# Kernel optimization log

Measured on AMD Instinct MI355X. Metric: run time of the kernel, lower is better.

Reference implementation:

```python
import jax, jax.numpy as jnp
import numpy as np

NUM_CAMS, NUM_LEVELS, NUM_PTS, NUM_GROUPS = 6, 4, 13, 8


def grid_sample(fm, grid):
    """Bilinear grid_sample, align_corners=False, zeros padding.
    fm: (N,C,H,W); grid: (N,P,Q,2) xy in [-1,1] -> (N,C,P,Q)."""
    N, C, H, W = fm.shape
    x, y = grid[..., 0], grid[..., 1]
    ix = ((x + 1.0) * W - 1.0) * 0.5
    iy = ((y + 1.0) * H - 1.0) * 0.5
    ix0f = jnp.floor(ix)
    iy0f = jnp.floor(iy)
    wx1 = ix - ix0f
    wy1 = iy - iy0f
    wx0 = 1.0 - wx1
    wy0 = 1.0 - wy1
    ix0 = ix0f.astype(jnp.int32)
    iy0 = iy0f.astype(jnp.int32)
    flat = fm.reshape(N, C, H * W)

    def gather(iyc, ixc):
        valid = ((ixc >= 0) & (ixc < W) & (iyc >= 0) & (iyc < H)).astype(fm.dtype)
        idx = jnp.clip(iyc, 0, H - 1) * W + jnp.clip(ixc, 0, W - 1)
        g = jnp.take_along_axis(flat, idx.reshape(N, 1, -1), axis=2)
        return g.reshape((N, C) + idx.shape[1:]) * valid[:, None]

    v00 = gather(iy0, ix0)
    v01 = gather(iy0, ix0 + 1)
    v10 = gather(iy0 + 1, ix0)
    v11 = gather(iy0 + 1, ix0 + 1)
    return (v00 * (wy0 * wx0)[:, None] + v01 * (wy0 * wx1)[:, None]
            + v10 * (wy1 * wx0)[:, None] + v11 * (wy1 * wx1)[:, None])


def setup_inputs() -> dict:
    key = jax.random.key(0)
    ks = jax.random.split(key, 16)
    bs, NA, E = 2, 900, 256
    shapes = [(12, E, 64, 176), (12, E, 32, 88), (12, E, 16, 44), (12, E, 8, 22)]
    proj = jnp.eye(4, dtype=jnp.float32)[None, None] + 0.1 * jax.random.normal(ks[0], (bs, NUM_CAMS, 4, 4), jnp.float32)
    return {
        "instance_feature": jax.random.normal(ks[1], (bs, NA, E), jnp.float32),
        "anchor": jax.random.normal(ks[2], (bs, NA, E), jnp.float32),
        "anchor_embed": jax.random.normal(ks[3], (bs, NA, E), jnp.float32),
        "fm0": jax.random.normal(ks[4], shapes[0], jnp.float32),
        "fm1": jax.random.normal(ks[5], shapes[1], jnp.float32),
        "fm2": jax.random.normal(ks[6], shapes[2], jnp.float32),
        "fm3": jax.random.normal(ks[7], shapes[3], jnp.float32),
        "projection_mat": proj,
        "W_kps": 0.02 * jax.random.normal(ks[8], (E, NUM_PTS * 3), jnp.float32),
        "b_kps": jnp.zeros((NUM_PTS * 3,), jnp.float32),
        "W_wfc": 0.02 * jax.random.normal(ks[9], (E, NUM_GROUPS * NUM_CAMS * NUM_LEVELS * NUM_PTS), jnp.float32),
        "b_wfc": jnp.zeros((NUM_GROUPS * NUM_CAMS * NUM_LEVELS * NUM_PTS,), jnp.float32),
        "W_out": 0.02 * jax.random.normal(ks[10], (E, E), jnp.float32),
        "b_out": jnp.zeros((E,), jnp.float32),
    }


def reference(instance_feature, anchor, anchor_embed, fm0, fm1, fm2, fm3,
              projection_mat, W_kps, b_kps, W_wfc, b_wfc, W_out, b_out):
    bs, NA, E = instance_feature.shape
    C, L, P, G = NUM_CAMS, NUM_LEVELS, NUM_PTS, NUM_GROUPS
    gd = E // G
    # key points: anchor center + learned offsets (kps_generator)
    offs = (instance_feature @ W_kps + b_kps).reshape(bs, NA, P, 3)
    key_points = anchor[:, :, None, :3] + offs  # (bs,NA,P,3)
    # fusion weights: softmax over cam*level*pt slots, per group
    feat = instance_feature + anchor_embed
    w = (feat @ W_wfc + b_wfc).reshape(bs, NA, C * L * P, G)
    w = jax.nn.softmax(w, axis=-2)
    # project points to 2D
    pts = jnp.concatenate([key_points, jnp.ones_like(key_points[..., :1])], axis=-1)
    p2d = jnp.einsum('bcij,bnpj->bcnpi', projection_mat, pts)  # (bs,C,NA,P,4)
    depth = 1.0 / jnp.clip(p2d[..., 2:3], 1e-5)
    grid = (p2d[..., :2] * depth).reshape(bs * C, NA, P, 2)
    # multi-level bilinear sampling
    samples = [grid_sample(fm, grid) for fm in (fm0, fm1, fm2, fm3)]  # (bs*C,E,NA,P)
    feats = jnp.concatenate(samples, axis=3)  # (bs*C,E,NA,L*P)
    feats = feats.reshape(bs, C, E, NA, L * P).transpose(0, 3, 1, 4, 2)
    feats = feats.reshape(bs, NA, C * L * P, E)
    # grouped weighted fusion over all cam/level/pt slots
    fused = (w[..., None] * feats.reshape(bs, NA, C * L * P, G, gd)).sum(axis=2)
    fused = fused.reshape(bs, NA, E)
    out = fused @ W_out + b_out
    return out + instance_feature
```

## Files before the change

### kernel.cpp

```cpp
#include <hip/hip_runtime.h>
#include <hip/hip_bf16.h>

#define C_NUM_CAMS 6
#define C_NUM_LEVELS 4
#define C_NUM_PTS 13
#define C_NUM_GROUPS 8
#define C_BS 2
#define C_NA 900
#define C_E 256
#define C_NSLOT 312
#define C_NCOL 2496
#define C_NANCH 1800

#define LB0 0
#define LB1 34603008
#define LB2 43253760
#define LB3 45416448
#define FM8_WS_BYTES 45957120ull
#define WGT_WS_BYTES 17971200ull
#define WBT_WS_BYTES 1277952ull

typedef float floatx2 __attribute__((ext_vector_type(2)));
typedef float f32x4 __attribute__((ext_vector_type(4)));
typedef short s16x8 __attribute__((ext_vector_type(8)));
typedef float f32x4v __attribute__((ext_vector_type(4)));

static __device__ __forceinline__ int pk_fp8(float a, float b, float c, float d) {
  int v = __builtin_amdgcn_cvt_pk_fp8_f32(a, b, 0, false);
  v = __builtin_amdgcn_cvt_pk_fp8_f32(c, d, v, true);
  return v;
}
static __device__ __forceinline__ unsigned short f2bf(float f) {
  __hip_bfloat16 h = __float2bfloat16(f);
  return *reinterpret_cast<unsigned short*>(&h);
}

__global__ __launch_bounds__(256) void dfa_prep_wbt(
    const float* __restrict__ W, unsigned short* __restrict__ Wbt) {
  int c = blockIdx.x;
  int d = threadIdx.x;
  Wbt[(size_t)c * 256 + d] = f2bf(W[(size_t)d * C_NCOL + c]);
}

__global__ __launch_bounds__(256) void dfa_transpose8(
    const float* __restrict__ fm0, const float* __restrict__ fm1,
    const float* __restrict__ fm2, const float* __restrict__ fm3,
    unsigned char* __restrict__ out) {
  int id = blockIdx.x;
  const float* fm;
  int HW, strips;
  long long base;
  int rem;
  if (id < 528)      { rem = id;       fm = fm0; HW = 11264; strips = 44; base = LB0; }
  else if (id < 660) { rem = id - 528; fm = fm1; HW = 2816;  strips = 11; base = LB1; }
  else if (id < 696) { rem = id - 660; fm = fm2; HW = 704;   strips = 3;  base = LB2; }
  else               { rem = id - 696; fm = fm3; HW = 176;   strips = 1;  base = LB3; }
  int img = rem / strips;
  int px0 = (rem % strips) * 256;

  __shared__ int lds[64][260];
  int t = threadIdx.x;
  int w = t >> 6, lane = t & 63;

  {
    int pxl = lane * 4;
    bool pv = (px0 + pxl) < HW;
    const float* src = fm + (size_t)img * 256 * HW + px0 + pxl;
    if (pv) {
#pragma unroll 4
      for (int cq = 0; cq < 16; ++cq) {
        int ch = w * 64 + cq * 4;
        const float* s = src + (size_t)ch * HW;
        f32x4 r0 = *(const f32x4*)(s);
        f32x4 r1 = *(const f32x4*)(s + HW);
        f32x4 r2 = *(const f32x4*)(s + 2 * (size_t)HW);
        f32x4 r3 = *(const f32x4*)(s + 3 * (size_t)HW);
        int4 o;
        o.x = pk_fp8(r0.x, r1.x, r2.x, r3.x);
        o.y = pk_fp8(r0.y, r1.y, r2.y, r3.y);
        o.z = pk_fp8(r0.z, r1.z, r2.z, r3.z);
        o.w = pk_fp8(r0.w, r1.w, r2.w, r3.w);
        *(int4*)&lds[w * 16 + cq][pxl] = o;
      }
    }
  }
  __syncthreads();
  {
    int cq16 = (lane & 15) * 4;
    int pxs = lane >> 4;
#pragma unroll 4
    for (int i = 0; i < 16; ++i) {
      int px = w * 64 + i * 4 + pxs;
      if (px0 + px < HW) {
        int4 o;
        o.x = lds[cq16 + 0][px];
        o.y = lds[cq16 + 1][px];
        o.z = lds[cq16 + 2][px];
        o.w = lds[cq16 + 3][px];
        *(int4*)(out + base + ((long long)img * HW + px0 + px) * 256 + cq16 * 4) = o;
      }
    }
  }
}

__global__ __launch_bounds__(256) void dfa_logits_mfma(
    const float* __restrict__ IF, const float* __restrict__ AE,
    const unsigned short* __restrict__ Wbt, const float* __restrict__ bwfc,
    float* __restrict__ logits) {
  int m0 = blockIdx.x * 128;
  int n0 = blockIdx.y * 128;
  int t = threadIdx.x;
  int w = t >> 6, lane = t & 63;

  __shared__ unsigned short As[128][40];
  __shared__ unsigned short Bs[128][40];

  f32x4v acc[4][4];
#pragma unroll
  for (int mi = 0; mi < 4; ++mi)
#pragma unroll
    for (int ni = 0; ni < 4; ++ni)
      acc[mi][ni] = (f32x4v){0.f, 0.f, 0.f, 0.f};

  int r = t >> 1;
  int half = (t & 1) * 16;
  int wr = (w >> 1) * 64, wc = (w & 1) * 64;
  int rsel = lane & 15;
  int koff = (lane >> 4) * 8;

  for (int ks = 0; ks < 8; ++ks) {
    int k0 = ks * 32;
    {
      int a = m0 + r;
      s16x8 o0 = {0, 0, 0, 0, 0, 0, 0, 0};
      s16x8 o1 = {0, 0, 0, 0, 0, 0, 0, 0};
      if (a < C_NANCH) {
        const float* pI = IF + (size_t)a * 256 + k0 + half;
        const float* pA = AE + (size_t)a * 256 + k0 + half;
        f32x4 i0 = *(const f32x4*)(pI + 0), i1 = *(const f32x4*)(pI + 4);
        f32x4 i2 = *(const f32x4*)(pI + 8), i3 = *(const f32x4*)(pI + 12);
        f32x4 a0 = *(const f32x4*)(pA + 0), a1 = *(const f32x4*)(pA + 4);
        f32x4 a2 = *(const f32x4*)(pA + 8), a3 = *(const f32x4*)(pA + 12);
        o0[0] = (short)f2bf(i0.x + a0.x); o0[1] = (short)f2bf(i0.y + a0.y);
        o0[2] = (short)f2bf(i0.z + a0.z); o0[3] = (short)f2bf(i0.w + a0.w);
        o0[4] = (short)f2bf(i1.x + a1.x); o0[5] = (short)f2bf(i1.y + a1.y);
        o0[6] = (short)f2bf(i1.z + a1.z); o0[7] = (short)f2bf(i1.w + a1.w);
        o1[0] = (short)f2bf(i2.x + a2.x); o1[1] = (short)f2bf(i2.y + a2.y);
        o1[2] = (short)f2bf(i2.z + a2.z); o1[3] = (short)f2bf(i2.w + a2.w);
        o1[4] = (short)f2bf(i3.x + a3.x); o1[5] = (short)f2bf(i3.y + a3.y);
        o1[6] = (short)f2bf(i3.z + a3.z); o1[7] = (short)f2bf(i3.w + a3.w);
      }
      *(s16x8*)&As[r][half] = o0;
      *(s16x8*)&As[r][half + 8] = o1;
    }
    {
      int c = n0 + r;
      s16x8 b0 = {0, 0, 0, 0, 0, 0, 0, 0};
      s16x8 b1 = {0, 0, 0, 0, 0, 0, 0, 0};
      if (c < C_NCOL) {
        const unsigned short* p = Wbt + (size_t)c * 256 + k0 + half;
        b0 = *(const s16x8*)(p);
        b1 = *(const s16x8*)(p + 8);
      }
      *(s16x8*)&Bs[r][half] = b0;
      *(s16x8*)&Bs[r][half + 8] = b1;
    }
    __syncthreads();

    s16x8 af[4], bf[4];
#pragma unroll
    for (int mi = 0; mi < 4; ++mi)
      af[mi] = *(const s16x8*)&As[wr + mi * 16 + rsel][koff];
#pragma unroll
    for (int ni = 0; ni < 4; ++ni)
      bf[ni] = *(const s16x8*)&Bs[wc + ni * 16 + rsel][koff];
#pragma unroll
    for (int mi = 0; mi < 4; ++mi)
#pragma unroll
      for (int ni = 0; ni < 4; ++ni)
        acc[mi][ni] = __builtin_amdgcn_mfma_f32_16x16x32_bf16(
            af[mi], bf[ni], acc[mi][ni], 0, 0, 0);
    __syncthreads();
  }

  int rowb = (lane >> 4) * 4;
  int colo = lane & 15;
#pragma unroll
  for (int ni = 0; ni < 4; ++ni) {
    int col = n0 + wc + ni * 16 + colo;
    if (col >= C_NCOL) continue;
    float bias = bwfc[col];
#pragma unroll
    for (int mi = 0; mi < 4; ++mi) {
#pragma unroll
      for (int j = 0; j < 4; ++j) {
        int row = m0 + wr + mi * 16 + rowb + j;
        if (row < C_NANCH)
          logits[(size_t)row * C_NCOL + col] = acc[mi][ni][j] + bias;
      }
    }
  }
}

__global__ __launch_bounds__(256) void dfa_agg_full(
    const unsigned char* __restrict__ fmws,
    const float* __restrict__ logits,
    const float* __restrict__ IF, const float* __restrict__ anchor,
    const float* __restrict__ Wkps, const float* __restrict__ bkps,
    const float* __restrict__ projm,
    const float* __restrict__ Wout, const float* __restrict__ bout,
    float* __restrict__ out) {
  int bn = blockIdx.x;
  int b = bn / C_NA;
  int t = threadIdx.x;
  int w = t >> 6, lane = t & 63;

  __shared__ __align__(16) float logitsS[8 * 312];
  __shared__ __align__(16) float swgt[C_NCOL];
  __shared__ unsigned short csS[1248];
  __shared__ __align__(16) float partS[8][256];
  __shared__ __align__(16) float fusedS[256];
  __shared__ float kpS[13][3];
  __shared__ float invS[8];

  int2* centry = (int2*)logitsS;
  float2* gridS = (float2*)fusedS;

  for (int i = t; i < C_NCOL; i += 256) {
    float v = logits[(size_t)bn * C_NCOL + i];
    logitsS[(i & 7) * 312 + (i >> 3)] = v;
  }
  __syncthreads();

  {
    int g = t >> 5, l32 = t & 31;
    float* row = logitsS + g * 312;
    float m = -1e30f;
    for (int s = l32; s < C_NSLOT; s += 32) m = fmaxf(m, row[s]);
#pragma unroll
    for (int off = 16; off; off >>= 1) m = fmaxf(m, __shfl_xor(m, off, 32));
    float sum = 0.f;
    for (int s = l32; s < C_NSLOT; s += 32) {
      float e = __expf(row[s] - m);
      row[s] = e;
      sum += e;
    }
#pragma unroll
    for (int off = 16; off; off >>= 1) sum += __shfl_xor(sum, off, 32);
    if (l32 == 0) invS[g] = 1.f / sum;
  }
  __syncthreads();

  for (int i = t; i < C_NCOL; i += 256)
    swgt[i] = logitsS[(i & 7) * 312 + (i >> 3)] * invS[i & 7];
  if (t < 39) {
    const float* f = IF + (size_t)bn * 256;
    float a0 = 0.f, a1 = 0.f, a2 = 0.f, a3 = 0.f;
    for (int d = 0; d < 256; d += 4) {
      a0 = fmaf(f[d + 0], Wkps[(d + 0) * 39 + t], a0);
      a1 = fmaf(f[d + 1], Wkps[(d + 1) * 39 + t], a1);
      a2 = fmaf(f[d + 2], Wkps[(d + 2) * 39 + t], a2);
      a3 = fmaf(f[d + 3], Wkps[(d + 3) * 39 + t], a3);
    }
    float acc = bkps[t] + ((a0 + a1) + (a2 + a3));
    int p = t / 3, ax = t % 3;
    kpS[p][ax] = anchor[(size_t)bn * 256 + ax] + acc;
  }
  __syncthreads();

  if (t < 78) {
    int c = t / 13, p = t % 13;
    const float* M = projm + (size_t)(b * 6 + c) * 16;
    float kx = kpS[p][0], ky = kpS[p][1], kz = kpS[p][2];
    float x = M[0] * kx + M[1] * ky + M[2] * kz + M[3];
    float y = M[4] * kx + M[5] * ky + M[6] * kz + M[7];
    float z = M[8] * kx + M[9] * ky + M[10] * kz + M[11];
    float zc = fmaxf(z, 1e-5f);
    float inv = 1.0f / zc;
    gridS[t] = make_float2(x * inv, y * inv);
  }
  __syncthreads();

  int cnt = 0;
  {
    int ebase = w * 312;
#pragma unroll
    for (int r = 0; r < 2; ++r) {
      int li = r * 64 + lane;
      bool lv = li < 78;
      int s = w * 78 + (lv ? li : 0);
      int cam = s / 52, rr = s % 52, l = rr / 13, p = rr % 13;
      float2 g2 = gridS[cam * 13 + p];
      int Wi = (l == 0) ? 176 : (l == 1) ? 88 : (l == 2) ? 44 : 22;
      int Hi = (l == 0) ? 64 : (l == 1) ? 32 : (l == 2) ? 16 : 8;
      float Wf = (float)Wi, Hf = (float)Hi;
      float ix = ((g2.x + 1.0f) * Wf - 1.0f) * 0.5f;
      float iy = ((g2.y + 1.0f) * Hf - 1.0f) * 0.5f;
      float ix0 = floorf(ix), iy0 = floorf(iy);
      float wx1 = ix - ix0, wy1 = iy - iy0;
      float wx0 = 1.f - wx1, wy0 = 1.f - wy1;
      bool vx0 = (ix0 >= 0.f) && (ix0 < Wf);
      bool vx1 = (ix0 + 1.f >= 0.f) && (ix0 + 1.f < Wf);
      bool vy0 = (iy0 >= 0.f) && (iy0 < Hf);
      bool vy1 = (iy0 + 1.f >= 0.f) && (iy0 + 1.f < Hf);
      int xi0 = (int)fminf(fmaxf(ix0, 0.f), Wf - 1.f);
      int xi1 = (int)fminf(fmaxf(ix0 + 1.f, 0.f), Wf - 1.f);
      int yi0 = (int)fminf(fmaxf(iy0, 0.f), Hf - 1.f);
      int yi1 = (int)fminf(fmaxf(iy0 + 1.f, 0.f), Hf - 1.f);
      int lb = (l == 0) ? LB0 : (l == 1) ? LB1 : (l == 2) ? LB2 : LB3;
      int ib = lb + (b * 6 + cam) * Wi * Hi * 256;
      float cw[4];
      int co[4];
      cw[0] = (vx0 && vy0) ? wy0 * wx0 : 0.f;
      cw[1] = (vx1 && vy0) ? wy0 * wx1 : 0.f;
      cw[2] = (vx0 && vy1) ? wy1 * wx0 : 0.f;
      cw[3] = (vx1 && vy1) ? wy1 * wx1 : 0.f;
      co[0] = ib + (yi0 * Wi + xi0) * 256;
      co[1] = ib + (yi0 * Wi + xi1) * 256;
      co[2] = ib + (yi1 * Wi + xi0) * 256;
      co[3] = ib + (yi1 * Wi + xi1) * 256;
      unsigned short sw8 = (unsigned short)(s * 8);
#pragma unroll
      for (int k = 0; k < 4; ++k) {
        bool v = lv && (cw[k] != 0.f);
        unsigned long long mb = __ballot(v);
        int pos = cnt + __popcll(mb & ((1ull << lane) - 1ull));
        if (v) {
          centry[ebase + pos] = make_int2(co[k], __float_as_int(cw[k]));
          csS[ebase + pos] = sw8;
        }
        cnt += (int)__popcll(mb);
      }
    }
    if (cnt & 1) {
      if (lane == 0) {
        centry[ebase + cnt] = make_int2(0, 0);
        csS[ebase + cnt] = 0;
      }
      cnt++;
    }
  }

  int half = lane >> 5, l32 = lane & 31;
  int ch = l32 * 8;
  int g = l32 >> 2;
  float acc[8];
#pragma unroll
  for (int j = 0; j < 8; ++j) acc[j] = 0.f;
  {
    int ebase = w * 312;
    int nIter = cnt >> 1;
#pragma unroll 8
    for (int i = 0; i < nIter; ++i) {
      int idx = ebase + 2 * i + half;
      int2 e = centry[idx];
      float wgt_s = swgt[(int)csS[idx] + g];
      float cw = __int_as_float(e.y) * wgt_s;
      int2 u = *reinterpret_cast<const int2*>(fmws + e.x + ch);
      floatx2 p0 = __builtin_amdgcn_cvt_pk_f32_fp8(u.x, false);
      floatx2 p1 = __builtin_amdgcn_cvt_pk_f32_fp8(u.x, true);
      floatx2 p2 = __builtin_amdgcn_cvt_pk_f32_fp8(u.y, false);
      floatx2 p3 = __builtin_amdgcn_cvt_pk_f32_fp8(u.y, true);
      acc[0] = fmaf(cw, p0.x, acc[0]);
      acc[1] = fmaf(cw, p0.y, acc[1]);
      acc[2] = fmaf(cw, p1.x, acc[2]);
      acc[3] = fmaf(cw, p1.y, acc[3]);
      acc[4] = fmaf(cw, p2.x, acc[4]);
      acc[5] = fmaf(cw, p2.y, acc[5]);
      acc[6] = fmaf(cw, p3.x, acc[6]);
      acc[7] = fmaf(cw, p3.y, acc[7]);
    }
  }
  {
    int row = w * 2 + half;
    float4 v0 = make_float4(acc[0], acc[1], acc[2], acc[3]);
    float4 v1 = make_float4(acc[4], acc[5], acc[6], acc[7]);
    *reinterpret_cast<float4*>(&partS[row][ch]) = v0;
    *reinterpret_cast<float4*>(&partS[row][ch + 4]) = v1;
  }
  __syncthreads();

  float fv = 0.f;
#pragma unroll
  for (int r = 0; r < 8; ++r) fv += partS[r][t];
  fusedS[t] = fv;
  __syncthreads();

  float o = bout[t] + IF[(size_t)bn * 256 + t];
#pragma unroll 8
  for (int d = 0; d < 256; ++d)
    o = fmaf(fusedS[d], Wout[d * 256 + t], o);
  out[(size_t)bn * 256 + t] = o;
}

__global__ __launch_bounds__(256) void dfa_logits_gemm_fb(
    const float* __restrict__ IF, const float* __restrict__ AE,
    const float* __restrict__ Wwfc, const float* __restrict__ bwfc,
    float* __restrict__ logits) {
  __shared__ float feat_t[256][16];
  int t = threadIdx.x;
  int a0 = blockIdx.x * 15;
  int col = blockIdx.y * 256 + t;
  bool cv = col < C_NCOL;
#pragma unroll
  for (int a = 0; a < 15; ++a) {
    int bn = a0 + a;
    feat_t[t][a] = IF[(size_t)bn * 256 + t] + AE[(size_t)bn * 256 + t];
  }
  feat_t[t][15] = 0.f;
  __syncthreads();
  float acc[15];
  float bias = cv ? bwfc[col] : 0.f;
#pragma unroll
  for (int a = 0; a < 15; ++a) acc[a] = bias;
  const float* wp = Wwfc + col;
#pragma unroll 8
  for (int d = 0; d < 256; ++d) {
    float wv = cv ? wp[(size_t)d * C_NCOL] : 0.f;
#pragma unroll
    for (int a = 0; a < 15; ++a) acc[a] = fmaf(feat_t[d][a], wv, acc[a]);
  }
  if (cv) {
#pragma unroll
    for (int a = 0; a < 15; ++a)
      logits[(size_t)(a0 + a) * C_NCOL + col] = acc[a];
  }
}

__global__ __launch_bounds__(256) void dfa_softmax(float* __restrict__ wgt) {
  int bn = blockIdx.x;
  float* w = wgt + (size_t)bn * C_NCOL;
  __shared__ float buf[C_NCOL];
  int t = threadIdx.x;
  for (int i = t; i < C_NCOL; i += 256) buf[i] = w[i];
  __syncthreads();
  int g = t >> 5, lane = t & 31;
  float m = -1e30f;
  for (int s = lane; s < C_NSLOT; s += 32) m = fmaxf(m, buf[s * 8 + g]);
#pragma unroll
  for (int off = 16; off; off >>= 1) m = fmaxf(m, __shfl_xor(m, off, 32));
  float sum = 0.f;
  for (int s = lane; s < C_NSLOT; s += 32) {
    float e = expf(buf[s * 8 + g] - m);
    buf[s * 8 + g] = e;
    sum += e;
  }
#pragma unroll
  for (int off = 16; off; off >>= 1) sum += __shfl_xor(sum, off, 32);
  float inv = 1.f / sum;
  for (int s = lane; s < C_NSLOT; s += 32) w[s * 8 + g] = buf[s * 8 + g] * inv;
}

__global__ __launch_bounds__(128) void dfa_points(
    const float* __restrict__ IF, const float* __restrict__ anchor,
    const float* __restrict__ Wkps, const float* __restrict__ bkps,
    const float* __restrict__ projm, float2* __restrict__ grid) {
  int bn = blockIdx.x;
  int b = bn / C_NA;
  int t = threadIdx.x;
  __shared__ float kp[13][3];
  if (t < 39) {
    float acc = bkps[t];
    const float* f = IF + (size_t)bn * 256;
    for (int d = 0; d < 256; ++d) acc = fmaf(f[d], Wkps[d * 39 + t], acc);
    int p = t / 3, ax = t % 3;
    kp[p][ax] = anchor[(size_t)bn * 256 + ax] + acc;
  }
  __syncthreads();
  if (t < 78) {
    int c = t / 13, p = t % 13;
    const float* M = projm + (size_t)(b * 6 + c) * 16;
    float kx = kp[p][0], ky = kp[p][1], kz = kp[p][2];
    float x = M[0] * kx + M[1] * ky + M[2] * kz + M[3];
    float y = M[4] * kx + M[5] * ky + M[6] * kz + M[7];
    float z = M[8] * kx + M[9] * ky + M[10] * kz + M[11];
    float zc = fmaxf(z, 1e-5f);
    float inv = 1.0f / zc;
    grid[(size_t)bn * 78 + t] = make_float2(x * inv, y * inv);
  }
}

struct __align__(16) SlotInfo { int o[4]; float w[4]; };

__global__ __launch_bounds__(256) void dfa_agg_fb(
    const float* __restrict__ fm0, const float* __restrict__ fm1,
    const float* __restrict__ fm2, const float* __restrict__ fm3,
    const float2* __restrict__ grid, const float* __restrict__ wgt,
    const float* __restrict__ IF, const float* __restrict__ Wout,
    const float* __restrict__ bout, float* __restrict__ out) {
  int bn = blockIdx.x;
  int b = bn / C_NA;
  int t = threadIdx.x;
  int w = t >> 6, lane = t & 63;

  __shared__ SlotInfo slot[C_NSLOT];
  __shared__ int sflag[C_NSLOT];
  __shared__ float swgt[C_NCOL];
  __shared__ float part[4][256];
  __shared__ float fused[256];

  for (int i = t; i < C_NCOL; i += 256) swgt[i] = wgt[(size_t)bn * C_NCOL + i];

  for (int s = t; s < C_NSLOT; s += 256) {
    int c = s / 52, r = s % 52, l = r / 13, p = r % 13;
    float2 g2 = grid[(size_t)bn * 78 + c * 13 + p];
    int Wi = (l == 0) ? 176 : (l == 1) ? 88 : (l == 2) ? 44 : 22;
    int Hi = (l == 0) ? 64 : (l == 1) ? 32 : (l == 2) ? 16 : 8;
    float Wf = (float)Wi, Hf = (float)Hi;
    float ix = ((g2.x + 1.0f) * Wf - 1.0f) * 0.5f;
    float iy = ((g2.y + 1.0f) * Hf - 1.0f) * 0.5f;
    float ix0 = floorf(ix), iy0 = floorf(iy);
    float wx1 = ix - ix0, wy1 = iy - iy0;
    float wx0 = 1.f - wx1, wy0 = 1.f - wy1;
    bool vx0 = (ix0 >= 0.f) && (ix0 < Wf);
    bool vx1 = (ix0 + 1.f >= 0.f) && (ix0 + 1.f < Wf);
    bool vy0 = (iy0 >= 0.f) && (iy0 < Hf);
    bool vy1 = (iy0 + 1.f >= 0.f) && (iy0 + 1.f < Hf);
    int xi0 = (int)fminf(fmaxf(ix0, 0.f), Wf - 1.f);
    int xi1 = (int)fminf(fmaxf(ix0 + 1.f, 0.f), Wf - 1.f);
    int yi0 = (int)fminf(fmaxf(iy0, 0.f), Hf - 1.f);
    int yi1 = (int)fminf(fmaxf(iy0 + 1.f, 0.f), Hf - 1.f);
    int img = b * 6 + c;
    int HW = Wi * Hi;
    SlotInfo si;
    int ib = img * 256 * HW;
    si.o[0] = ib + yi0 * Wi + xi0;
    si.o[1] = ib + yi0 * Wi + xi1;
    si.o[2] = ib + yi1 * Wi + xi0;
    si.o[3] = ib + yi1 * Wi + xi1;
    si.w[0] = (vx0 && vy0) ? wy0 * wx0 : 0.f;
    si.w[1] = (vx1 && vy0) ? wy0 * wx1 : 0.f;
    si.w[2] = (vx0 && vy1) ? wy1 * wx0 : 0.f;
    si.w[3] = (vx1 && vy1) ? wy1 * wx1 : 0.f;
    slot[s] = si;
    sflag[s] = (si.w[0] + si.w[1] + si.w[2] + si.w[3] == 0.f) ? -1 : l;
  }
  __syncthreads();

  int g = lane >> 3;
  int ch = lane * 4;
  float4 acc = make_float4(0.f, 0.f, 0.f, 0.f);
  for (int s = w; s < C_NSLOT; s += 4) {
    int fl = sflag[s];
    if (fl < 0) continue;
    SlotInfo si = slot[s];
    float wg = swgt[s * 8 + g];
    const float* fp = (fl == 0) ? fm0 : (fl == 1) ? fm1 : (fl == 2) ? fm2 : fm3;
    int HW = (fl == 0) ? 11264 : (fl == 1) ? 2816 : (fl == 2) ? 704 : 176;
    float4 sv = make_float4(0.f, 0.f, 0.f, 0.f);
#pragma unroll
    for (int k = 0; k < 4; ++k) {
      if (si.w[k] != 0.f) {
        sv.x = fmaf(si.w[k], fp[si.o[k] + (size_t)(ch + 0) * HW], sv.x);
        sv.y = fmaf(si.w[k], fp[si.o[k] + (size_t)(ch + 1) * HW], sv.y);
        sv.z = fmaf(si.w[k], fp[si.o[k] + (size_t)(ch + 2) * HW], sv.z);
        sv.w = fmaf(si.w[k], fp[si.o[k] + (size_t)(ch + 3) * HW], sv.w);
      }
    }
    acc.x = fmaf(sv.x, wg, acc.x);
    acc.y = fmaf(sv.y, wg, acc.y);
    acc.z = fmaf(sv.z, wg, acc.z);
    acc.w = fmaf(sv.w, wg, acc.w);
  }
  *reinterpret_cast<float4*>(&part[w][ch]) = acc;
  __syncthreads();

  fused[t] = part[0][t] + part[1][t] + part[2][t] + part[3][t];
  __syncthreads();

  float o = bout[t] + IF[(size_t)bn * 256 + t];
#pragma unroll 4
  for (int d = 0; d < 256; ++d)
    o = fmaf(fused[d], Wout[d * 256 + t], o);
  out[(size_t)bn * 256 + t] = o;
}

extern "C" void kernel_launch(void* const* d_in, const int* in_sizes, int n_in,
                              void* d_out, int out_size, void* d_ws, size_t ws_size,
                              hipStream_t stream) {
  const float* IF     = (const float*)d_in[0];
  const float* anchor = (const float*)d_in[1];
  const float* AE     = (const float*)d_in[2];
  const float* fm0    = (const float*)d_in[3];
  const float* fm1    = (const float*)d_in[4];
  const float* fm2    = (const float*)d_in[5];
  const float* fm3    = (const float*)d_in[6];
  const float* projm  = (const float*)d_in[7];
  const float* Wkps   = (const float*)d_in[8];
  const float* bkps   = (const float*)d_in[9];
  const float* Wwfc   = (const float*)d_in[10];
  const float* bwfc   = (const float*)d_in[11];
  const float* Wout   = (const float*)d_in[12];
  const float* bout   = (const float*)d_in[13];
  float* out = (float*)d_out;
  char* ws = (char*)d_ws;

  bool full = ws_size >= (FM8_WS_BYTES + WGT_WS_BYTES + WBT_WS_BYTES);
  if (full) {
    unsigned char* fmws = (unsigned char*)ws;
    float* wgt = (float*)(ws + FM8_WS_BYTES);
    unsigned short* wbt = (unsigned short*)(ws + FM8_WS_BYTES + WGT_WS_BYTES);
    dfa_prep_wbt<<<C_NCOL, 256, 0, stream>>>(Wwfc, wbt);
    dfa_transpose8<<<708, 256, 0, stream>>>(fm0, fm1, fm2, fm3, fmws);
    dfa_logits_mfma<<<dim3(15, 20), 256, 0, stream>>>(IF, AE, wbt, bwfc, wgt);
    dfa_agg_full<<<1800, 256, 0, stream>>>(fmws, wgt, IF, anchor, Wkps, bkps,
                                           projm, Wout, bout, out);
  } else {
    float* wgt  = (float*)ws;
    float2* grd = (float2*)(ws + WGT_WS_BYTES);
    dfa_logits_gemm_fb<<<dim3(120, 10), 256, 0, stream>>>(IF, AE, Wwfc, bwfc, wgt);
    dfa_softmax<<<1800, 256, 0, stream>>>(wgt);
    dfa_points<<<1800, 128, 0, stream>>>(IF, anchor, Wkps, bkps, projm, grd);
    dfa_agg_fb<<<1800, 256, 0, stream>>>(fm0, fm1, fm2, fm3, grd, wgt,
                                         IF, Wout, bout, out);
  }
}
```

Baseline: 130.1 us.

## Tile W transpose through LDS and merge fm transpose with logits GEMM launch

Rewrites the weight transpose/bf16 conversion to use 64-column LDS tiles with vectorized coalesced reads and writes instead of one strided scalar load per thread. Merges the fp8 feature-map transpose kernel and the logits MFMA GEMM into a single launch that dispatches by block index, so the two independent stages can run concurrently and one launch boundary disappears. The merged kernel reserves the larger shared-memory footprint for all blocks, which may reduce occupancy for the GEMM blocks.

Result: faster. 121.8 us (-6.4%).

```diff
diff --git a/kernel.cpp b/kernel.cpp
--- a/kernel.cpp
+++ b/kernel.cpp
@@ -37,166 +37,186 @@
 
 __global__ __launch_bounds__(256) void dfa_prep_wbt(
     const float* __restrict__ W, unsigned short* __restrict__ Wbt) {
-  int c = blockIdx.x;
-  int d = threadIdx.x;
-  Wbt[(size_t)c * 256 + d] = f2bf(W[(size_t)d * C_NCOL + c]);
-}
-
-__global__ __launch_bounds__(256) void dfa_transpose8(
+  __shared__ unsigned short tile[64][264];
+  int t = threadIdx.x;
+  int c0 = blockIdx.x * 64;
+  int rA = t >> 4;
+  int cA = (t & 15) * 4;
+#pragma unroll
+  for (int p = 0; p < 16; ++p) {
+    int r = p * 16 + rA;
+    f32x4 v = *(const f32x4*)(W + (size_t)r * C_NCOL + c0 + cA);
+    tile[cA + 0][r] = f2bf(v.x);
+    tile[cA + 1][r] = f2bf(v.y);
+    tile[cA + 2][r] = f2bf(v.z);
+    tile[cA + 3][r] = f2bf(v.w);
+  }
+  __syncthreads();
+  int cB = t >> 5;
+  int i4 = t & 31;
+#pragma unroll
+  for (int p = 0; p < 8; ++p) {
+    int c = p * 8 + cB;
+    int4 o = *(const int4*)&tile[c][i4 * 8];
+    *(int4*)(Wbt + (size_t)(c0 + c) * 256 + i4 * 8) = o;
+  }
+}
+
+__global__ __launch_bounds__(256) void dfa_stage1(
     const float* __restrict__ fm0, const float* __restrict__ fm1,
     const float* __restrict__ fm2, const float* __restrict__ fm3,
-    unsigned char* __restrict__ out) {
-  int id = blockIdx.x;
-  const float* fm;
-  int HW, strips;
-  long long base;
-  int rem;
-  if (id < 528)      { rem = id;       fm = fm0; HW = 11264; strips = 44; base = LB0; }
-  else if (id < 660) { rem = id - 528; fm = fm1; HW = 2816;  strips = 11; base = LB1; }
-  else if (id < 696) { rem = id - 660; fm = fm2; HW = 704;   strips = 3;  base = LB2; }
-  else               { rem = id - 696; fm = fm3; HW = 176;   strips = 1;  base = LB3; }
-  int img = rem / strips;
-  int px0 = (rem % strips) * 256;
-
-  __shared__ int lds[64][260];
-  int t = threadIdx.x;
-  int w = t >> 6, lane = t & 63;
-
-  {
-    int pxl = lane * 4;
-    bool pv = (px0 + pxl) < HW;
-    const float* src = fm + (size_t)img * 256 * HW + px0 + pxl;
-    if (pv) {
-#pragma unroll 4
-      for (int cq = 0; cq < 16; ++cq) {
-        int ch = w * 64 + cq * 4;
-        const float* s = src + (size_t)ch * HW;
-        f32x4 r0 = *(const f32x4*)(s);
-        f32x4 r1 = *(const f32x4*)(s + HW);
-        f32x4 r2 = *(const f32x4*)(s + 2 * (size_t)HW);
-        f32x4 r3 = *(const f32x4*)(s + 3 * (size_t)HW);
-        int4 o;
-        o.x = pk_fp8(r0.x, r1.x, r2.x, r3.x);
-        o.y = pk_fp8(r0.y, r1.y, r2.y, r3.y);
-        o.z = pk_fp8(r0.z, r1.z, r2.z, r3.z);
-        o.w = pk_fp8(r0.w, r1.w, r2.w, r3.w);
-        *(int4*)&lds[w * 16 + cq][pxl] = o;
-      }
-    }
-  }
-  __syncthreads();
-  {
-    int cq16 = (lane & 15) * 4;
-    int pxs = lane >> 4;
-#pragma unroll 4
-    for (int i = 0; i < 16; ++i) {
-      int px = w * 64 + i * 4 + pxs;
-      if (px0 + px < HW) {
-        int4 o;
-        o.x = lds[cq16 + 0][px];
-        o.y = lds[cq16 + 1][px];
-        o.z = lds[cq16 + 2][px];
-        o.w = lds[cq16 + 3][px];
-        *(int4*)(out + base + ((long long)img * HW + px0 + px) * 256 + cq16 * 4) = o;
-      }
-    }
-  }
-}
-
-__global__ __launch_bounds__(256) void dfa_logits_mfma(
+    unsigned char* __restrict__ outw,
     const float* __restrict__ IF, const float* __restrict__ AE,
     const unsigned short* __restrict__ Wbt, const float* __restrict__ bwfc,
     float* __restrict__ logits) {
-  int m0 = blockIdx.x * 128;
-  int n0 = blockIdx.y * 128;
+  __shared__ __align__(16) char smem[66560];
+  int id = blockIdx.x;
   int t = threadIdx.x;
   int w = t >> 6, lane = t & 63;
 
-  __shared__ unsigned short As[128][40];
-  __shared__ unsigned short Bs[128][40];
-
-  f32x4v acc[4][4];
-#pragma unroll
-  for (int mi = 0; mi < 4; ++mi)
-#pragma unroll
-    for (int ni = 0; ni < 4; ++ni)
-      acc[mi][ni] = (f32x4v){0.f, 0.f, 0.f, 0.f};
-
-  int r = t >> 1;
-  int half = (t & 1) * 16;
-  int wr = (w >> 1) * 64, wc = (w & 1) * 64;
-  int rsel = lane & 15;
-  int koff = (lane >> 4) * 8;
-
-  for (int ks = 0; ks < 8; ++ks) {
-    int k0 = ks * 32;
+  if (id < 708) {
+    int (*lds)[260] = (int(*)[260])smem;
+    const float* fm;
+    int HW, strips;
+    long long base;
+    int rem;
+    if (id < 528)      { rem = id;       fm = fm0; HW = 11264; strips = 44; base = LB0; }
+    else if (id < 660) { rem = id - 528; fm = fm1; HW = 2816;  strips = 11; base = LB1; }
+    else if (id < 696) { rem = id - 660; fm = fm2; HW = 704;   strips = 3;  base = LB2; }
+    else               { rem = id - 696; fm = fm3; HW = 176;   strips = 1;  base = LB3; }
+    int img = rem / strips;
+    int px0 = (rem % strips) * 256;
+
     {
-      int a = m0 + r;
-      s16x8 o0 = {0, 0, 0, 0, 0, 0, 0, 0};
-      s16x8 o1 = {0, 0, 0, 0, 0, 0, 0, 0};
-      if (a < C_NANCH) {
-        const float* pI = IF + (size_t)a * 256 + k0 + half;
-        const float* pA = AE + (size_t)a * 256 + k0 + half;
-        f32x4 i0 = *(const f32x4*)(pI + 0), i1 = *(const f32x4*)(pI + 4);
-        f32x4 i2 = *(const f32x4*)(pI + 8), i3 = *(const f32x4*)(pI + 12);
-        f32x4 a0 = *(const f32x4*)(pA + 0), a1 = *(const f32x4*)(pA + 4);
-        f32x4 a2 = *(const f32x4*)(pA + 8), a3 = *(const f32x4*)(pA + 12);
-        o0[0] = (short)f2bf(i0.x + a0.x); o0[1] = (short)f2bf(i0.y + a0.y);
-        o0[2] = (short)f2bf(i0.z + a0.z); o0[3] = (short)f2bf(i0.w + a0.w);
-        o0[4] = (short)f2bf(i1.x + a1.x); o0[5] = (short)f2bf(i1.y + a1.y);
-        o0[6] = (short)f2bf(i1.z + a1.z); o0[7] = (short)f2bf(i1.w + a1.w);
-        o1[0] = (short)f2bf(i2.x + a2.x); o1[1] = (short)f2bf(i2.y + a2.y);
-        o1[2] = (short)f2bf(i2.z + a2.z); o1[3] = (short)f2bf(i2.w + a2.w);
-        o1[4] = (short)f2bf(i3.x + a3.x); o1[5] = (short)f2bf(i3.y + a3.y);
-        o1[6] = (short)f2bf(i3.z + a3.z); o1[7] = (short)f2bf(i3.w + a3.w);
-      }
-      *(s16x8*)&As[r][half] = o0;
-      *(s16x8*)&As[r][half + 8] = o1;
-    }
+      int pxl = lane * 4;
+      bool pv = (px0 + pxl) < HW;
+      const float* src = fm + (size_t)img * 256 * HW + px0 + pxl;
+      if (pv) {
+#pragma unroll 4
+        for (int cq = 0; cq < 16; ++cq) {
+          int ch = w * 64 + cq * 4;
+          const float* s = src + (size_t)ch * HW;
+          f32x4 r0 = *(const f32x4*)(s);
+          f32x4 r1 = *(const f32x4*)(s + HW);
+          f32x4 r2 = *(const f32x4*)(s + 2 * (size_t)HW);
+          f32x4 r3 = *(const f32x4*)(s + 3 * (size_t)HW);
+          int4 o;
+          o.x = pk_fp8(r0.x, r1.x, r2.x, r3.x);
+          o.y = pk_fp8(r0.y, r1.y, r2.y, r3.y);
+          o.z = pk_fp8(r0.z, r1.z, r2.z, r3.z);
+          o.w = pk_fp8(r0.w, r1.w, r2.w, r3.w);
+          *(int4*)&lds[w * 16 + cq][pxl] = o;
+        }
+      }
+    }
+    __syncthreads();
     {
-      int c = n0 + r;
-      s16x8 b0 = {0, 0, 0, 0, 0, 0, 0, 0};
-      s16x8 b1 = {0, 0, 0, 0, 0, 0, 0, 0};
-      if (c < C_NCOL) {
-        const unsigned short* p = Wbt + (size_t)c * 256 + k0 + half;
-        b0 = *(const s16x8*)(p);
-        b1 = *(const s16x8*)(p + 8);
-      }
-      *(s16x8*)&Bs[r][half] = b0;
-      *(s16x8*)&Bs[r][half + 8] = b1;
-    }
-    __syncthreads();
-
-    s16x8 af[4], bf[4];
+      int cq16 = (lane & 15) * 4;
+      int pxs = lane >> 4;
+#pragma unroll 4
+      for (int i = 0; i < 16; ++i) {
+        int px = w * 64 + i * 4 + pxs;
+        if (px0 + px < HW) {
+          int4 o;
+          o.x = lds[cq16 + 0][px];
+          o.y = lds[cq16 + 1][px];
+          o.z = lds[cq16 + 2][px];
+          o.w = lds[cq16 + 3][px];
+          *(int4*)(outw + base + ((long long)img * HW + px0 + px) * 256 + cq16 * 4) = o;
+        }
+      }
+    }
+  } else {
+    typedef unsigned short us40[40];
+    us40* As = (us40*)smem;
+    us40* Bs = (us40*)(smem + 10240);
+    int rem = id - 708;
+    int m0 = (rem % 15) * 128;
+    int n0 = (rem / 15) * 128;
+
+    f32x4v acc[4][4];
 #pragma unroll
     for (int mi = 0; mi < 4; ++mi)
-      af[mi] = *(const s16x8*)&As[wr + mi * 16 + rsel][koff];
-#pragma unroll
-    for (int ni = 0; ni < 4; ++ni)
-      bf[ni] = *(const s16x8*)&Bs[wc + ni * 16 + rsel][koff];
-#pragma unroll
-    for (int mi = 0; mi < 4; ++mi)
 #pragma unroll
       for (int ni = 0; ni < 4; ++ni)
-        acc[mi][ni] = __builtin_amdgcn_mfma_f32_16x16x32_bf16(
-            af[mi], bf[ni], acc[mi][ni], 0, 0, 0);
-    __syncthreads();
-  }
-
-  int rowb = (lane >> 4) * 4;
-  int colo = lane & 15;
-#pragma unroll
-  for (int ni = 0; ni < 4; ++ni) {
-    int col = n0 + wc + ni * 16 + colo;
-    if (col >= C_NCOL) continue;
-    float bias = bwfc[col];
-#pragma unroll
-    for (int mi = 0; mi < 4; ++mi) {
-#pragma unroll
-      for (int j = 0; j < 4; ++j) {
-        int row = m0 + wr + mi * 16 + rowb + j;
-        if (row < C_NANCH)
-          logits[(size_t)row * C_NCOL + col] = acc[mi][ni][j] + bias;
+        acc[mi][ni] = (f32x4v){0.f, 0.f, 0.f, 0.f};
+
+    int r = t >> 1;
+    int half = (t & 1) * 16;
+    int wr = (w >> 1) * 64, wc = (w & 1) * 64;
+    int rsel = lane & 15;
+    int koff = (lane >> 4) * 8;
+
+    for (int ks = 0; ks < 8; ++ks) {
+      int k0 = ks * 32;
+      {
+        int a = m0 + r;
+        s16x8 o0 = {0, 0, 0, 0, 0, 0, 0, 0};
+        s16x8 o1 = {0, 0, 0, 0, 0, 0, 0, 0};
+        if (a < C_NANCH) {
+          const float* pI = IF + (size_t)a * 256 + k0 + half;
+          const float* pA = AE + (size_t)a * 256 + k0 + half;
+          f32x4 i0 = *(const f32x4*)(pI + 0), i1 = *(const f32x4*)(pI + 4);
+          f32x4 i2 = *(const f32x4*)(pI + 8), i3 = *(const f32x4*)(pI + 12);
+          f32x4 a0 = *(const f32x4*)(pA + 0), a1 = *(const f32x4*)(pA + 4);
+          f32x4 a2 = *(const f32x4*)(pA + 8), a3 = *(const f32x4*)(pA + 12);
+          o0[0] = (short)f2bf(i0.x + a0.x); o0[1] = (short)f2bf(i0.y + a0.y);
+          o0[2] = (short)f2bf(i0.z + a0.z); o0[3] = (short)f2bf(i0.w + a0.w);
+          o0[4] = (short)f2bf(i1.x + a1.x); o0[5] = (short)f2bf(i1.y + a1.y);
+          o0[6] = (short)f2bf(i1.z + a1.z); o0[7] = (short)f2bf(i1.w + a1.w);
+          o1[0] = (short)f2bf(i2.x + a2.x); o1[1] = (short)f2bf(i2.y + a2.y);
+          o1[2] = (short)f2bf(i2.z + a2.z); o1[3] = (short)f2bf(i2.w + a2.w);
+          o1[4] = (short)f2bf(i3.x + a3.x); o1[5] = (short)f2bf(i3.y + a3.y);
+          o1[6] = (short)f2bf(i3.z + a3.z); o1[7] = (short)f2bf(i3.w + a3.w);
+        }
+        *(s16x8*)&As[r][half] = o0;
+        *(s16x8*)&As[r][half + 8] = o1;
+      }
+      {
+        int c = n0 + r;
+        s16x8 b0 = {0, 0, 0, 0, 0, 0, 0, 0};
+        s16x8 b1 = {0, 0, 0, 0, 0, 0, 0, 0};
+        if (c < C_NCOL) {
+          const unsigned short* p = Wbt + (size_t)c * 256 + k0 + half;
+          b0 = *(const s16x8*)(p);
+          b1 = *(const s16x8*)(p + 8);
+        }
+        *(s16x8*)&Bs[r][half] = b0;
+        *(s16x8*)&Bs[r][half + 8] = b1;
+      }
+      __syncthreads();
+
+      s16x8 af[4], bf[4];
+#pragma unroll
+      for (int mi = 0; mi < 4; ++mi)
+        af[mi] = *(const s16x8*)&As[wr + mi * 16 + rsel][koff];
+#pragma unroll
+      for (int ni = 0; ni < 4; ++ni)
+        bf[ni] = *(const s16x8*)&Bs[wc + ni * 16 + rsel][koff];
+#pragma unroll
+      for (int mi = 0; mi < 4; ++mi)
+#pragma unroll
+        for (int ni = 0; ni < 4; ++ni)
+          acc[mi][ni] = __builtin_amdgcn_mfma_f32_16x16x32_bf16(
+              af[mi], bf[ni], acc[mi][ni], 0, 0, 0);
+      __syncthreads();
+    }
+
+    int rowb = (lane >> 4) * 4;
+    int colo = lane & 15;
+#pragma unroll
+    for (int ni = 0; ni < 4; ++ni) {
+      int col = n0 + wc + ni * 16 + colo;
+      if (col >= C_NCOL) continue;
+      float bias = bwfc[col];
+#pragma unroll
+      for (int mi = 0; mi < 4; ++mi) {
+#pragma unroll
+        for (int j = 0; j < 4; ++j) {
+          int row = m0 + wr + mi * 16 + rowb + j;
+          if (row < C_NANCH)
+            logits[(size_t)row * C_NCOL + col] = acc[mi][ni][j] + bias;
+        }
       }
     }
   }
@@ -600,9 +620,9 @@
     unsigned char* fmws = (unsigned char*)ws;
     float* wgt = (float*)(ws + FM8_WS_BYTES);
     unsigned short* wbt = (unsigned short*)(ws + FM8_WS_BYTES + WGT_WS_BYTES);
-    dfa_prep_wbt<<<C_NCOL, 256, 0, stream>>>(Wwfc, wbt);
-    dfa_transpose8<<<708, 256, 0, stream>>>(fm0, fm1, fm2, fm3, fmws);
-    dfa_logits_mfma<<<dim3(15, 20), 256, 0, stream>>>(IF, AE, wbt, bwfc, wgt);
+    dfa_prep_wbt<<<39, 256, 0, stream>>>(Wwfc, wbt);
+    dfa_stage1<<<1008, 256, 0, stream>>>(fm0, fm1, fm2, fm3, fmws,
+                                         IF, AE, wbt, bwfc, wgt);
     dfa_agg_full<<<1800, 256, 0, stream>>>(fmws, wgt, IF, anchor, Wkps, bkps,
                                            projm, Wout, bout, out);
   } else {
```
